# Performance work log

Hardware: AMD Instinct MI355X
Metric: run time of the kernel (lower is better)

## Reference

```python
import jax, jax.numpy as jnp
import numpy as np

N, E, Q = 50000, 500000, 100000
IN_DIM, HID, EDGE_DIM, NUM_CLASSES = 128, 128, 16, 2


def _glorot(key, shape):
    fan_in, fan_out = shape
    lim = (6.0 / (fan_in + fan_out)) ** 0.5
    return jax.random.uniform(key, shape, jnp.float32, -lim, lim)


def setup_inputs() -> dict:
    key = jax.random.key(0)
    ks = jax.random.split(key, 12)
    return {
        "node_feature": jax.random.normal(ks[0], (N, IN_DIM), jnp.float32),
        "edge_index": jax.random.randint(ks[1], (2, E), 0, N, jnp.int64),
        "edge_feature": jax.random.normal(ks[2], (E, EDGE_DIM), jnp.float32),
        "edge_label_index": jax.random.randint(ks[3], (2, Q), 0, N, jnp.int64),
        # conv1 params
        "c1_pre_W": _glorot(ks[4], (IN_DIM, IN_DIM)),
        "c1_pre_b": jnp.zeros((IN_DIM,), jnp.float32),
        "c1_msg_W": _glorot(ks[5], (2 * IN_DIM + EDGE_DIM, HID)),
        "c1_msg_b": jnp.zeros((HID,), jnp.float32),
        # conv2 params
        "c2_pre_W": _glorot(ks[6], (HID, HID)),
        "c2_pre_b": jnp.zeros((HID,), jnp.float32),
        "c2_msg_W": _glorot(ks[7], (2 * HID + EDGE_DIM, HID)),
        "c2_msg_b": jnp.zeros((HID,), jnp.float32),
        # link-prediction head
        "lp_W": _glorot(ks[8], (2 * HID, NUM_CLASSES)),
        "lp_b": jnp.zeros((NUM_CLASSES,), jnp.float32),
    }


def _mlp_message_conv(x, edge_index, edge_feature, pre_W, pre_b, msg_W, msg_b):
    # pre_conv: Linear + ReLU
    h = jax.nn.relu(x @ pre_W + pre_b)
    src, dst = edge_index[0], edge_index[1]
    # PyG default flow source_to_target: x_i = target, x_j = source
    x_i = h[dst]  # [E, d]
    x_j = h[src]  # [E, d]
    msg = jnp.concatenate([x_i, x_j, edge_feature], axis=1) @ msg_W + msg_b  # [E, out]
    # aggr='add' onto target nodes
    return jax.ops.segment_sum(msg, dst, num_segments=x.shape[0])


def reference(node_feature, edge_index, edge_feature, edge_label_index,
              c1_pre_W, c1_pre_b, c1_msg_W, c1_msg_b,
              c2_pre_W, c2_pre_b, c2_msg_W, c2_msg_b,
              lp_W, lp_b):
    # eval mode: dropout is identity
    x = jax.nn.relu(_mlp_message_conv(node_feature, edge_index, edge_feature,
                                      c1_pre_W, c1_pre_b, c1_msg_W, c1_msg_b))
    x = _mlp_message_conv(x, edge_index, edge_feature,
                          c2_pre_W, c2_pre_b, c2_msg_W, c2_msg_b)
    nodes_first = x[edge_label_index[0]]   # [Q, hid]
    nodes_second = x[edge_label_index[1]]  # [Q, hid]
    pred = jnp.concatenate([nodes_first, nodes_second], axis=-1) @ lp_W + lp_b
    return pred
```

## Files before the change

### kernel.cpp

```cpp
#include <hip/hip_runtime.h>
#include <cstdint>
#include <cstddef>


typedef __attribute__((ext_vector_type(8))) short short8;
typedef __attribute__((ext_vector_type(4))) float float4v;

__device__ __forceinline__ ushort f2b(float f) {
    uint u = __float_as_uint(f);
    u = u + 0x7fff + ((u >> 16) & 1);
    return (ushort)(u >> 16);
}
__device__ __forceinline__ float b2f(ushort h) {
    return __uint_as_float(((uint)h) << 16);
}
__device__ __forceinline__ uint pack2(float a, float b) {
    return (uint)f2b(a) | ((uint)f2b(b) << 16);
}

#define F_MSG     1
#define F_RELU    2
#define F_DEGBIAS 4
#define F_OUTB    8
#define F_IN32    16
#define F_HEAD    32

#define XS_STRIDE 72

__launch_bounds__(256, 2)
__global__ void gemm_mfma(const ushort* __restrict__ A, const ushort* __restrict__ B,
                          const ushort* __restrict__ EF, const float* __restrict__ A32,
                          const float* __restrict__ DEG, const ushort* __restrict__ Wt,
                          const float* __restrict__ bias, ushort* __restrict__ outB,
                          const float* __restrict__ lpW, float* __restrict__ z,
                          int M, int Kp, int flags)
{
    __shared__ ushort xs[128 * XS_STRIDE];
    __shared__ ushort ws[128 * XS_STRIDE];
    const int tid  = threadIdx.x;
    const int lane = tid & 63;
    const int wave = tid >> 6;
    const int row0 = blockIdx.x << 7;

    float4v acc[2][8];
#pragma unroll
    for (int m = 0; m < 2; ++m)
#pragma unroll
        for (int t = 0; t < 8; ++t) acc[m][t] = (float4v){0.f, 0.f, 0.f, 0.f};

    const int arow0 = (wave << 5) + (lane & 15);
    const int koff  = (lane >> 4) << 3;
    const int bcol  = lane & 15;

    for (int kt = 0; kt < Kp; kt += 64) {
        __syncthreads();
        for (int idx = tid; idx < 128 * 8; idx += 256) {
            const int n = idx >> 3;
            const int g = idx & 7;
            const uint4 v = *(const uint4*)&Wt[(size_t)n * Kp + kt + (g << 3)];
            *(uint4*)&ws[n * XS_STRIDE + (g << 3)] = v;
        }
        if (flags & F_MSG) {
            for (int idx = tid; idx < 128 * 8; idx += 256) {
                const int r  = idx >> 3;
                const int g  = idx & 7;
                const int gr = row0 + r;
                const int kk = kt + (g << 3);
                uint4 v = make_uint4(0, 0, 0, 0);
                if (gr < M) {
                    if (kk < 128) {
                        uint4 a = *(const uint4*)&A[((size_t)gr << 7) + kk];
                        const float d = DEG[gr];
                        uint* p = (uint*)&a;
#pragma unroll
                        for (int q = 0; q < 4; ++q)
                            p[q] = pack2(b2f((ushort)(p[q] & 0xffff)) * d,
                                         b2f((ushort)(p[q] >> 16)) * d);
                        v = a;
                    } else if (kk < 256) {
                        v = *(const uint4*)&B[((size_t)gr << 7) + kk - 128];
                    } else if (kk < 272) {
                        v = *(const uint4*)&EF[((size_t)gr << 4) + kk - 256];
                    }
                }
                *(uint4*)&xs[r * XS_STRIDE + (g << 3)] = v;
            }
        } else if (flags & F_IN32) {
            for (int idx = tid; idx < 128 * 8; idx += 256) {
                const int r  = idx >> 3;
                const int g  = idx & 7;
                const int gr = row0 + r;
                uint4 v = make_uint4(0, 0, 0, 0);
                if (gr < M) {
                    const float4 f0 = *(const float4*)&A32[((size_t)gr << 7) + kt + (g << 3)];
                    const float4 f1 = *(const float4*)&A32[((size_t)gr << 7) + kt + (g << 3) + 4];
                    v.x = pack2(f0.x, f0.y); v.y = pack2(f0.z, f0.w);
                    v.z = pack2(f1.x, f1.y); v.w = pack2(f1.z, f1.w);
                }
                *(uint4*)&xs[r * XS_STRIDE + (g << 3)] = v;
            }
        } else {
            for (int idx = tid; idx < 128 * 8; idx += 256) {
                const int r  = idx >> 3;
                const int g  = idx & 7;
                const int gr = row0 + r;
                uint4 v = make_uint4(0, 0, 0, 0);
                if (gr < M) v = *(const uint4*)&A[((size_t)gr << 7) + kt + (g << 3)];
                *(uint4*)&xs[r * XS_STRIDE + (g << 3)] = v;
            }
        }
        __syncthreads();
#pragma unroll
        for (int s = 0; s < 64; s += 32) {
            const short8 a0 = *(const short8*)&xs[arow0 * XS_STRIDE + s + koff];
            const short8 a1 = *(const short8*)&xs[(arow0 + 16) * XS_STRIDE + s + koff];
#pragma unroll
            for (int t = 0; t < 8; ++t) {
                const short8 bf = *(const short8*)&ws[((t << 4) + bcol) * XS_STRIDE + s + koff];
                acc[0][t] = __builtin_amdgcn_mfma_f32_16x16x32_bf16(a0, bf, acc[0][t], 0, 0, 0);
                acc[1][t] = __builtin_amdgcn_mfma_f32_16x16x32_bf16(a1, bf, acc[1][t], 0, 0, 0);
            }
        }
    }

    float bcv[8];
#pragma unroll
    for (int t = 0; t < 8; ++t) bcv[t] = bias[(t << 4) + bcol];

    if (flags & F_HEAD) {
        const float2* lw = (const float2*)lpW;
        float2 wa[8], wb[8];
#pragma unroll
        for (int t = 0; t < 8; ++t) {
            const int col = (t << 4) + bcol;
            wa[t] = lw[col];
            wb[t] = lw[128 + col];
        }
#pragma unroll
        for (int m = 0; m < 2; ++m) {
            const int rbase = row0 + (wave << 5) + (m << 4) + ((lane >> 4) << 2);
#pragma unroll
            for (int r = 0; r < 4; ++r) {
                const int row = rbase + r;
                const float d = (row < M) ? DEG[row] : 0.f;
                float za0 = 0.f, za1 = 0.f, zb0 = 0.f, zb1 = 0.f;
#pragma unroll
                for (int t = 0; t < 8; ++t) {
                    const float v = acc[m][t][r] + d * bcv[t];
                    za0 += v * wa[t].x; za1 += v * wa[t].y;
                    zb0 += v * wb[t].x; zb1 += v * wb[t].y;
                }
#pragma unroll
                for (int mk = 8; mk > 0; mk >>= 1) {
                    za0 += __shfl_xor(za0, mk);
                    za1 += __shfl_xor(za1, mk);
                    zb0 += __shfl_xor(zb0, mk);
                    zb1 += __shfl_xor(zb1, mk);
                }
                if (bcol == 0 && row < M)
                    *(float4*)&z[(size_t)row * 4] = make_float4(za0, za1, zb0, zb1);
            }
        }
    } else {
#pragma unroll
        for (int m = 0; m < 2; ++m) {
            const int rbase = row0 + (wave << 5) + (m << 4) + ((lane >> 4) << 2);
#pragma unroll
            for (int t = 0; t < 8; ++t) {
                const int col = (t << 4) + bcol;
#pragma unroll
                for (int r = 0; r < 4; ++r) {
                    const int row = rbase + r;
                    if (row >= M) continue;
                    float v = acc[m][t][r];
                    v += (flags & F_DEGBIAS) ? DEG[row] * bcv[t] : bcv[t];
                    if (flags & F_RELU) v = fmaxf(v, 0.f);
                    outB[((size_t)row << 7) + col] = f2b(v);
                }
            }
        }
    }
}

__launch_bounds__(256)
__global__ void prep(const float* __restrict__ c1pW, const float* __restrict__ c2pW,
                     const float* __restrict__ c1mW, const float* __restrict__ c2mW,
                     ushort* __restrict__ wtp1, ushort* __restrict__ wtp2,
                     ushort* __restrict__ wtm1, ushort* __restrict__ wtm2,
                     int* __restrict__ counts, int N)
{
    const int gtid = blockIdx.x * 256 + threadIdx.x;
    const int gstr = gridDim.x * 256;
    for (int i = gtid; i < N; i += gstr) counts[i] = 0;
    for (int idx = gtid; idx < 128 * 128; idx += gstr) {
        const int n = idx >> 7, k = idx & 127;
        wtp1[idx] = f2b(c1pW[(size_t)k * 128 + n]);
        wtp2[idx] = f2b(c2pW[(size_t)k * 128 + n]);
    }
    for (int idx = gtid; idx < 128 * 320; idx += gstr) {
        const int n = idx / 320, k = idx - n * 320;
        wtm1[idx] = (k < 272) ? f2b(c1mW[(size_t)k * 128 + n]) : (ushort)0;
        wtm2[idx] = (k < 272) ? f2b(c2mW[(size_t)k * 128 + n]) : (ushort)0;
    }
}

__launch_bounds__(256)
__global__ void hist_kernel(const int* __restrict__ ei, int* __restrict__ counts, int E)
{
    const int e = blockIdx.x * 256 + threadIdx.x;
    if (e < E) atomicAdd(&counts[ei[E + e]], 1);
}

__launch_bounds__(256)
__global__ void scan_phase1(const int* __restrict__ counts, int* __restrict__ rowstart,
                            int* __restrict__ blocksums, int N)
{
    __shared__ int sdata[256];
    const int t = threadIdx.x;
    const int i = blockIdx.x * 256 + t;
    const int v = (i < N) ? counts[i] : 0;
    sdata[t] = v;
    __syncthreads();
    for (int off = 1; off < 256; off <<= 1) {
        const int add = (t >= off) ? sdata[t - off] : 0;
        __syncthreads();
        sdata[t] += add;
        __syncthreads();
    }
    if (i < N) rowstart[i] = sdata[t] - v;
    if (t == 255) blocksums[blockIdx.x] = sdata[255];
}

__launch_bounds__(256)
__global__ void scan_phase23(const int* __restrict__ counts, const int* __restrict__ bs,
                             int* __restrict__ rowstart, int* __restrict__ cursor,
                             float* __restrict__ degf, int N, int E)
{
    __shared__ int sdata[256];
    const int t = threadIdx.x;
    const int vb = blockIdx.x;
    int part = 0;
    for (int j = t; j < vb; j += 256) part += bs[j];
    sdata[t] = part;
    __syncthreads();
    for (int s = 128; s > 0; s >>= 1) {
        if (t < s) sdata[t] += sdata[t + s];
        __syncthreads();
    }
    const int off = sdata[0];
    const int i = vb * 256 + t;
    if (i < N) {
        const int rs = rowstart[i] + off;
        rowstart[i] = rs;
        cursor[i]   = rs;
        degf[i]     = (float)counts[i];
    }
    if (vb == 0 && t == 0) rowstart[N] = E;
}

__launch_bounds__(256)
__global__ void build_elist(const int* __restrict__ ei, int* __restrict__ cursor,
                            int2* __restrict__ elist, int E)
{
    const int e = blockIdx.x * 256 + threadIdx.x;
    if (e >= E) return;
    const int d = ei[E + e];
    const int pos = atomicAdd(&cursor[d], 1);
    elist[pos] = make_int2(ei[e], e);
}

__launch_bounds__(256)
__global__ void gather(const int2* __restrict__ elist, const int* __restrict__ rowstart,
                       const ushort* __restrict__ h, ushort* __restrict__ agg,
                       const float* __restrict__ ef, ushort* __restrict__ aggef,
                       int N, int doEf)
{
    const int tid = threadIdx.x;
    if (doEf) {
        const int nvb = (N + 15) / 16;
        const int lane16 = tid & 15;
        for (int vb = blockIdx.x; vb < nvb; vb += gridDim.x) {
            const int node = vb * 16 + (tid >> 4);
            if (node >= N) continue;
            const int beg = rowstart[node];
            const int end = rowstart[node + 1];
            float acc = 0.f;
            for (int k = beg; k < end; ++k)
                acc += ef[((size_t)elist[k].y << 4) + lane16];
            aggef[((size_t)node << 4) + lane16] = f2b(acc);
        }
    }
    {
        const int nvb = (N + 7) / 8;
        const int grp = tid >> 5;
        const int l   = tid & 31;
        for (int vb = blockIdx.x; vb < nvb; vb += gridDim.x) {
            const int node = vb * 8 + grp;
            if (node >= N) continue;
            const int beg = rowstart[node];
            const int end = rowstart[node + 1];
            float a0 = 0.f, a1 = 0.f, a2 = 0.f, a3 = 0.f;
            int k = beg;
            for (; k + 7 < end; k += 8) {
                uint2 v[8];
#pragma unroll
                for (int j = 0; j < 8; ++j) {
                    const int s = elist[k + j].x;
                    v[j] = *(const uint2*)&h[((size_t)s << 7) + (l << 2)];
                }
#pragma unroll
                for (int j = 0; j < 8; ++j) {
                    a0 += b2f((ushort)(v[j].x & 0xffff));
                    a1 += b2f((ushort)(v[j].x >> 16));
                    a2 += b2f((ushort)(v[j].y & 0xffff));
                    a3 += b2f((ushort)(v[j].y >> 16));
                }
            }
            for (; k < end; ++k) {
                const uint2 v = *(const uint2*)&h[((size_t)elist[k].x << 7) + (l << 2)];
                a0 += b2f((ushort)(v.x & 0xffff));
                a1 += b2f((ushort)(v.x >> 16));
                a2 += b2f((ushort)(v.y & 0xffff));
                a3 += b2f((ushort)(v.y >> 16));
            }
            uint2 o;
            o.x = pack2(a0, a1);
            o.y = pack2(a2, a3);
            *(uint2*)&agg[((size_t)node << 7) + (l << 2)] = o;
        }
    }
}

__launch_bounds__(256)
__global__ void head_kernel(const float4* __restrict__ z, const int* __restrict__ eli,
                            const float* __restrict__ lpb, float* __restrict__ out, int Q)
{
    const int q = blockIdx.x * 256 + threadIdx.x;
    if (q >= Q) return;
    const int a = eli[q];
    const int b = eli[Q + q];
    const float4 za = z[a];
    const float4 zb = z[b];
    float2 o = make_float2(za.x + zb.z + lpb[0], za.y + zb.w + lpb[1]);
    *(float2*)&out[(size_t)q * 2] = o;
}

extern "C" void kernel_launch(void* const* d_in, const int* in_sizes, int n_in,
                              void* d_out, int out_size, void* d_ws, size_t ws_size,
                              hipStream_t stream)
{
    const float* nf   = (const float*)d_in[0];
    const int*   ei   = (const int*)d_in[1];
    const float* ef   = (const float*)d_in[2];
    const int*   eli  = (const int*)d_in[3];
    const float* c1pW = (const float*)d_in[4];
    const float* c1pb = (const float*)d_in[5];
    const float* c1mW = (const float*)d_in[6];
    const float* c1mb = (const float*)d_in[7];
    const float* c2pW = (const float*)d_in[8];
    const float* c2pb = (const float*)d_in[9];
    const float* c2mW = (const float*)d_in[10];
    const float* c2mb = (const float*)d_in[11];
    const float* lpW  = (const float*)d_in[12];
    const float* lpb  = (const float*)d_in[13];
    float* out = (float*)d_out;

    const int N = in_sizes[0] / 128;
    const int E = in_sizes[1] / 2;
    const int Q = in_sizes[3] / 2;

    float* DEG = (float*)d_ws;
    float* z   = DEG + N;
    int* counts    = (int*)(z + (size_t)N * 4);
    int* rowstart  = counts + N;
    int* cursor    = rowstart + N + 1;
    int* blocksums = cursor + N;
    uintptr_t ep8 = (uintptr_t)(blocksums + 1024);
    ep8 = (ep8 + 7) & ~(uintptr_t)7;
    int2* elist = (int2*)ep8;
    uintptr_t up = (uintptr_t)(elist + E);
    up = (up + 15) & ~(uintptr_t)15;
    ushort* h_bf   = (ushort*)up;
    ushort* agg_bf = h_bf   + (size_t)N * 128;
    ushort* x1_bf  = agg_bf + (size_t)N * 128;
    ushort* ef_bf  = x1_bf  + (size_t)N * 128;
    ushort* wtp1   = ef_bf  + (size_t)N * 16;
    ushort* wtm1   = wtp1 + 128 * 128;
    ushort* wtp2   = wtm1 + 128 * 320;
    ushort* wtm2   = wtp2 + 128 * 128;

    const int gemmGrid = (N + 127) / 128;
    const int eGrid    = (E + 255) / 256;
    const int nGrid    = (N + 255) / 256;
    const int gGrid    = (N + 7) / 8;
    const int headGrid = (Q + 255) / 256;

    prep<<<nGrid, 256, 0, stream>>>(c1pW, c2pW, c1mW, c2mW, wtp1, wtp2, wtm1, wtm2,
                                    counts, N);
    hist_kernel<<<eGrid, 256, 0, stream>>>(ei, counts, E);
    scan_phase1<<<nGrid, 256, 0, stream>>>(counts, rowstart, blocksums, N);
    scan_phase23<<<nGrid, 256, 0, stream>>>(counts, blocksums, rowstart, cursor, DEG, N, E);
    build_elist<<<eGrid, 256, 0, stream>>>(ei, cursor, elist, E);

    gemm_mfma<<<gemmGrid, 256, 0, stream>>>(nullptr, nullptr, nullptr, nf, DEG, wtp1,
                                            c1pb, h_bf, nullptr, nullptr, N, 128,
                                            F_RELU | F_OUTB | F_IN32);
    gather<<<gGrid, 256, 0, stream>>>(elist, rowstart, h_bf, agg_bf, ef, ef_bf, N, 1);
    gemm_mfma<<<gemmGrid, 256, 0, stream>>>(h_bf, agg_bf, ef_bf, nullptr, DEG, wtm1,
                                            c1mb, x1_bf, nullptr, nullptr, N, 320,
                                            F_MSG | F_RELU | F_DEGBIAS | F_OUTB);

    gemm_mfma<<<gemmGrid, 256, 0, stream>>>(x1_bf, nullptr, nullptr, nullptr, DEG, wtp2,
                                            c2pb, h_bf, nullptr, nullptr, N, 128,
                                            F_RELU | F_OUTB);
    gather<<<gGrid, 256, 0, stream>>>(elist, rowstart, h_bf, agg_bf, nullptr, nullptr, N, 0);
    gemm_mfma<<<gemmGrid, 256, 0, stream>>>(h_bf, agg_bf, ef_bf, nullptr, DEG, wtm2,
                                            c2mb, nullptr, lpW, z, N, 320,
                                            F_MSG | F_DEGBIAS | F_HEAD);

    head_kernel<<<headGrid, 256, 0, stream>>>((const float4*)z, eli, lpb, out, Q);
}
```

Baseline: 323.9 us.

## Fuse edge-feature and neighbor gathers with 16-lane groups and shuffled indices

The gather kernel now uses 16 lanes per node with 16-byte loads instead of 32 lanes with 8-byte loads. Each group loads up to 16 edge-list entries cooperatively and broadcasts them with shuffles. The edge-feature aggregation is folded into the same loop instead of a separate pass over the CSR. This removes the redundant second traversal and the per-lane elist loads, at the cost of more registers and cross-lane shuffles.

New measurement: 316.7 us. 1.02x faster.

```diff
diff --git a/kernel.cpp b/kernel.cpp
--- a/kernel.cpp
+++ b/kernel.cpp
@@ -276,58 +276,72 @@
                        int N, int doEf)
 {
     const int tid = threadIdx.x;
-    if (doEf) {
-        const int nvb = (N + 15) / 16;
-        const int lane16 = tid & 15;
-        for (int vb = blockIdx.x; vb < nvb; vb += gridDim.x) {
-            const int node = vb * 16 + (tid >> 4);
-            if (node >= N) continue;
-            const int beg = rowstart[node];
-            const int end = rowstart[node + 1];
-            float acc = 0.f;
-            for (int k = beg; k < end; ++k)
-                acc += ef[((size_t)elist[k].y << 4) + lane16];
-            aggef[((size_t)node << 4) + lane16] = f2b(acc);
-        }
-    }
-    {
-        const int nvb = (N + 7) / 8;
-        const int grp = tid >> 5;
-        const int l   = tid & 31;
-        for (int vb = blockIdx.x; vb < nvb; vb += gridDim.x) {
-            const int node = vb * 8 + grp;
-            if (node >= N) continue;
-            const int beg = rowstart[node];
-            const int end = rowstart[node + 1];
-            float a0 = 0.f, a1 = 0.f, a2 = 0.f, a3 = 0.f;
-            int k = beg;
-            for (; k + 7 < end; k += 8) {
-                uint2 v[8];
-#pragma unroll
-                for (int j = 0; j < 8; ++j) {
-                    const int s = elist[k + j].x;
-                    v[j] = *(const uint2*)&h[((size_t)s << 7) + (l << 2)];
-                }
-#pragma unroll
-                for (int j = 0; j < 8; ++j) {
-                    a0 += b2f((ushort)(v[j].x & 0xffff));
-                    a1 += b2f((ushort)(v[j].x >> 16));
-                    a2 += b2f((ushort)(v[j].y & 0xffff));
-                    a3 += b2f((ushort)(v[j].y >> 16));
-                }
-            }
-            for (; k < end; ++k) {
-                const uint2 v = *(const uint2*)&h[((size_t)elist[k].x << 7) + (l << 2)];
+    const int grp = tid >> 4;
+    const int l   = tid & 15;
+    const int nvb = (N + 15) / 16;
+    for (int vb = blockIdx.x; vb < nvb; vb += gridDim.x) {
+        const int node = vb * 16 + grp;
+        if (node >= N) continue;
+        const int beg = rowstart[node];
+        const int end = rowstart[node + 1];
+        float a0 = 0.f, a1 = 0.f, a2 = 0.f, a3 = 0.f;
+        float a4 = 0.f, a5 = 0.f, a6 = 0.f, a7 = 0.f;
+        float efacc = 0.f;
+        int k = beg;
+        while (k < end) {
+            const int cnt = min(16, end - k);
+            const int2 ep = elist[k + min(l, cnt - 1)];
+            int j = 0;
+            for (; j + 8 <= cnt; j += 8) {
+                uint4 v[8];
+                float efv[8];
+#pragma unroll
+                for (int jj = 0; jj < 8; ++jj) {
+                    const int s = __shfl(ep.x, j + jj, 16);
+                    v[jj] = *(const uint4*)&h[((size_t)s << 7) + (l << 3)];
+                    if (doEf) {
+                        const int y = __shfl(ep.y, j + jj, 16);
+                        efv[jj] = ef[((size_t)y << 4) + l];
+                    }
+                }
+#pragma unroll
+                for (int jj = 0; jj < 8; ++jj) {
+                    a0 += b2f((ushort)(v[jj].x & 0xffff));
+                    a1 += b2f((ushort)(v[jj].x >> 16));
+                    a2 += b2f((ushort)(v[jj].y & 0xffff));
+                    a3 += b2f((ushort)(v[jj].y >> 16));
+                    a4 += b2f((ushort)(v[jj].z & 0xffff));
+                    a5 += b2f((ushort)(v[jj].z >> 16));
+                    a6 += b2f((ushort)(v[jj].w & 0xffff));
+                    a7 += b2f((ushort)(v[jj].w >> 16));
+                    if (doEf) efacc += efv[jj];
+                }
+            }
+            for (; j < cnt; ++j) {
+                const int s = __shfl(ep.x, j, 16);
+                const uint4 v = *(const uint4*)&h[((size_t)s << 7) + (l << 3)];
+                if (doEf) {
+                    const int y = __shfl(ep.y, j, 16);
+                    efacc += ef[((size_t)y << 4) + l];
+                }
                 a0 += b2f((ushort)(v.x & 0xffff));
                 a1 += b2f((ushort)(v.x >> 16));
                 a2 += b2f((ushort)(v.y & 0xffff));
                 a3 += b2f((ushort)(v.y >> 16));
-            }
-            uint2 o;
-            o.x = pack2(a0, a1);
-            o.y = pack2(a2, a3);
-            *(uint2*)&agg[((size_t)node << 7) + (l << 2)] = o;
-        }
+                a4 += b2f((ushort)(v.z & 0xffff));
+                a5 += b2f((ushort)(v.z >> 16));
+                a6 += b2f((ushort)(v.w & 0xffff));
+                a7 += b2f((ushort)(v.w >> 16));
+            }
+            k += cnt;
+        }
+        uint4 o;
+        o.x = pack2(a0, a1);
+        o.y = pack2(a2, a3);
+        o.z = pack2(a4, a5);
+        o.w = pack2(a6, a7);
+        *(uint4*)&agg[((size_t)node << 7) + (l << 3)] = o;
+        if (doEf) aggef[((size_t)node << 4) + l] = f2b(efacc);
     }
 }
 
@@ -392,7 +406,7 @@
     const int gemmGrid = (N + 127) / 128;
     const int eGrid    = (E + 255) / 256;
     const int nGrid    = (N + 255) / 256;
-    const int gGrid    = (N + 7) / 8;
+    const int gGrid    = (N + 15) / 16;
     const int headGrid = (Q + 255) / 256;
 
     prep<<<nGrid, 256, 0, stream>>>(c1pW, c2pW, c1mW, c2mW, wtp1, wtp2, wtm1, wtm2,
```
